# Kernel optimization log

Hardware: AMD Instinct MI355X
Metric: run time of the kernel (lower is better)

## Reference

```python
import jax, jax.numpy as jnp
import numpy as np

B, C_L_IN, C_L_OUT, C_J = 512, 64, 64, 16


def setup_inputs() -> dict:
    key = jax.random.key(0)
    ks = jax.random.split(key, 8)
    std = 0.02 / C_L_IN ** 0.5
    return {
        "F_in": jax.random.normal(ks[0], (B, C_L_IN, 4, 4), jnp.float32),
        "theta": jax.random.normal(ks[1], (B, C_J), jnp.float32),
        "W_bias": std * jax.random.normal(ks[2], (C_L_OUT, C_L_IN, 4, 4), jnp.float32),
        "W_cos": std * jax.random.normal(ks[3], (C_L_OUT, C_L_IN, C_J, 4, 4), jnp.float32),
        "W_sin": std * jax.random.normal(ks[4], (C_L_OUT, C_L_IN, C_J, 4, 4), jnp.float32),
        "Wb_bias": std * jax.random.normal(ks[5], (C_L_OUT, C_L_IN, 4, 4), jnp.float32),
        "Wb_cos": std * jax.random.normal(ks[6], (C_L_OUT, C_L_IN, C_J, 4, 4), jnp.float32),
        "Wb_sin": std * jax.random.normal(ks[7], (C_L_OUT, C_L_IN, C_J, 4, 4), jnp.float32),
    }


def reference(F_in, theta, W_bias, W_cos, W_sin, Wb_bias, Wb_cos, Wb_sin):
    cos_t = jnp.cos(theta)  # (B, C_J)
    sin_t = jnp.sin(theta)
    # U, Ub: (B, C_L_out, C_L_in, 4, 4)
    U = (W_bias
         + jnp.einsum('jicpq,bc->bjipq', W_cos, cos_t)
         + jnp.einsum('jicpq,bc->bjipq', W_sin, sin_t))
    Ub = (Wb_bias
          + jnp.einsum('jicpq,bc->bjipq', Wb_cos, cos_t)
          + jnp.einsum('jicpq,bc->bjipq', Wb_sin, sin_t))
    term1 = jnp.einsum('bipq,bjiqr->bjpr', F_in, U)
    term2 = jnp.einsum('bjipq,biqr->bjpr', Ub, F_in)
    return term1 + term2
```

## Files before the change

kernel.cpp:

```cpp
#include <hip/hip_runtime.h>


#define NRO_B   512
#define NRO_CL  64
#define K_DIM   8448
#define M_DIM   2048
#define N_DIM   256
#define SK      8
#define B_ELems  ((size_t)N_DIM * K_DIM)
#define FV_ELems ((size_t)M_DIM * N_DIM)
#define P_ELems  ((size_t)2 * SK * M_DIM * N_DIM)

typedef __attribute__((ext_vector_type(8))) _Float16 half8;
typedef __attribute__((ext_vector_type(4))) _Float16 half4_t;
typedef __attribute__((ext_vector_type(4))) float floatx4;

__device__ __forceinline__ void load16(const float* p, float w[4][4]) {
    const float4* p4 = (const float4*)p;
    #pragma unroll
    for (int a = 0; a < 4; ++a) {
        float4 x = p4[a];
        w[a][0] = x.x; w[a][1] = x.y; w[a][2] = x.z; w[a][3] = x.w;
    }
}

__device__ __forceinline__ half8 scale8(half8 v, _Float16 s) {
    half8 r;
    #pragma unroll
    for (int x = 0; x < 8; ++x) r[x] = v[x] * s;
    return r;
}

__global__ __launch_bounds__(256) void nro_prep(
    const float* __restrict__ F_in,
    const float* __restrict__ W_bias, const float* __restrict__ W_cos,
    const float* __restrict__ W_sin,  const float* __restrict__ Wb_bias,
    const float* __restrict__ Wb_cos, const float* __restrict__ Wb_sin,
    _Float16* __restrict__ Bbuf,
    _Float16* __restrict__ Fv)
{
    const int w = threadIdx.x >> 6, i = threadIdx.x & 63;
    if (blockIdx.x < 128) {
        const int b = blockIdx.x * 4 + w;
        float f[4][4];
        load16(F_in + ((size_t)b * 64 + i) * 16, f);
        #pragma unroll
        for (int a = 0; a < 4; ++a) {
            half4_t v0 = { (_Float16)f[a][0], (_Float16)f[a][1],
                           (_Float16)f[a][2], (_Float16)f[a][3] };
            *(half4_t*)(Fv + (size_t)(b * 4 + a) * 256 + i * 4) = v0;
            half4_t v1 = { (_Float16)f[0][a], (_Float16)f[1][a],
                           (_Float16)f[2][a], (_Float16)f[3][a] };
            *(half4_t*)(Fv + FV_ELems + (size_t)(b * 4 + a) * 256 + i * 4) = v1;
        }
    } else {
        const int unit = (blockIdx.x - 128) * 4 + w;
        const int j = unit >> 5, c = (unit >> 1) & 15, h = unit & 1;
        _Float16* Bd = Bbuf + (size_t)h * B_ELems;
        const size_t wbase = (((size_t)(j * 64 + i)) * 16 + c) * 16;

        float wc4[4][4], ws4[4][4];
        if (h == 0) { load16(W_cos  + wbase, wc4); load16(W_sin  + wbase, ws4); }
        else        { load16(Wb_cos + wbase, wc4); load16(Wb_sin + wbase, ws4); }

        const int gc  = (1 + c)  * 8 + (i >> 3);
        const int gs  = (17 + c) * 8 + (i >> 3);
        const int kin = (i & 7) * 4;
        #pragma unroll
        for (int a = 0; a < 4; ++a) {
            const int n = j * 4 + a;
            half4_t vc, vs;
            if (h == 0) {
                vc = (half4_t){ (_Float16)wc4[0][a], (_Float16)wc4[1][a],
                                (_Float16)wc4[2][a], (_Float16)wc4[3][a] };
                vs = (half4_t){ (_Float16)ws4[0][a], (_Float16)ws4[1][a],
                                (_Float16)ws4[2][a], (_Float16)ws4[3][a] };
            } else {
                vc = (half4_t){ (_Float16)wc4[a][0], (_Float16)wc4[a][1],
                                (_Float16)wc4[a][2], (_Float16)wc4[a][3] };
                vs = (half4_t){ (_Float16)ws4[a][0], (_Float16)ws4[a][1],
                                (_Float16)ws4[a][2], (_Float16)ws4[a][3] };
            }
            *(half4_t*)(Bd + ((size_t)gc * 256 + n) * 32 + kin) = vc;
            *(half4_t*)(Bd + ((size_t)gs * 256 + n) * 32 + kin) = vs;
        }
        if (c == 0) {
            float t[4][4];
            load16(((h == 0) ? W_bias : Wb_bias) + ((size_t)(j * 64 + i)) * 16, t);
            #pragma unroll
            for (int a = 0; a < 4; ++a) {
                half4_t v;
                if (h == 0) v = (half4_t){ (_Float16)t[0][a], (_Float16)t[1][a],
                                           (_Float16)t[2][a], (_Float16)t[3][a] };
                else        v = (half4_t){ (_Float16)t[a][0], (_Float16)t[a][1],
                                           (_Float16)t[a][2], (_Float16)t[a][3] };
                *(half4_t*)(Bd + ((size_t)(i >> 3) * 256 + (j * 4 + a)) * 32 + kin) = v;
            }
        }
    }
}

__global__ __launch_bounds__(512, 4) void nro_gemm(
    const _Float16* __restrict__ Bbuf, const _Float16* __restrict__ Fv,
    const float* __restrict__ theta,
    float* __restrict__ part)
{
    const int zs = blockIdx.x;
    const int z  = zs >> 3;
    const int sk = zs & 7;
    const int m0 = blockIdx.y * 128;

    const _Float16* Bm = Bbuf + (size_t)z * B_ELems;
    const _Float16* Fm = Fv + (size_t)z * FV_ELems + (size_t)m0 * 256;

    __shared__ _Float16 Fs[128 * 264];
    __shared__ float    trig[32 * 34];

    const int tid  = threadIdx.x;
    const int lane = tid & 63;
    const int w    = tid >> 6;
    const int wm   = (w >> 2) * 64;
    const int wn   = (w & 3) * 64;

    #pragma unroll
    for (int kk = 0; kk < 8; ++kk) {
        const int idx = kk * 512 + tid;
        const int row = idx >> 5, cf = idx & 31;
        half8 v = *(const half8*)(Fm + (size_t)row * 256 + cf * 8);
        *(half8*)(Fs + row * 264 + cf * 8) = v;
    }
    {
        const int bl = tid >> 4, c = tid & 15;
        const float th = theta[(m0 >> 2) * 16 + tid];
        trig[bl * 34 + 1 + c]  = __cosf(th);
        trig[bl * 34 + 17 + c] = __sinf(th);
        if (c == 0) trig[bl * 34] = 1.0f;
    }
    __syncthreads();

    const int fr = lane & 15, fq8 = (lane >> 4) * 8;

    const _Float16* Brow[4];
    #pragma unroll
    for (int t = 0; t < 4; ++t)
        Brow[t] = Bm + (size_t)(wn + t * 16 + fr) * 32 + fq8;

    floatx4 acc[4][4] = {};
    _Float16 tv[4] = {};

    int g = sk * 33;
    for (int kt = 0; kt < 33; ++kt, ++g) {
        const int cp  = g >> 3;
        const int iq0 = (g & 7) * 32;
        if (kt == 0 || (g & 7) == 0) {
            #pragma unroll
            for (int t = 0; t < 4; ++t)
                tv[t] = (_Float16)trig[((wm >> 2) + t * 4 + (fr >> 2)) * 34 + cp];
        }
        half8 bf[4];
        #pragma unroll
        for (int t = 0; t < 4; ++t)
            bf[t] = *(const half8*)(Brow[t] + (size_t)g * 8192);
        half8 af[4];
        #pragma unroll
        for (int t = 0; t < 4; ++t) {
            half8 fvf = *(const half8*)(Fs + (wm + t * 16 + fr) * 264 + iq0 + fq8);
            af[t] = scale8(fvf, tv[t]);
        }
        #pragma unroll
        for (int mt = 0; mt < 4; ++mt)
            #pragma unroll
            for (int nt = 0; nt < 4; ++nt)
                acc[mt][nt] = __builtin_amdgcn_mfma_f32_16x16x32_f16(
                    af[mt], bf[nt], acc[mt][nt], 0, 0, 0);
    }

    const int col = lane & 15, row4 = (lane >> 4) * 4;
    #pragma unroll
    for (int mt = 0; mt < 4; ++mt)
        #pragma unroll
        for (int nt = 0; nt < 4; ++nt)
            #pragma unroll
            for (int e = 0; e < 4; ++e) {
                const int m = m0 + wm + mt * 16 + row4 + e;
                const int n = wn + nt * 16 + col;
                part[((size_t)zs * M_DIM + m) * N_DIM + n] = acc[mt][nt][e];
            }
}

__global__ __launch_bounds__(256) void nro_reduce(
    const float* __restrict__ part, float* __restrict__ out)
{
    const int t = blockIdx.x * 256 + threadIdx.x;
    const int b = t >> 8;
    const int j = (t >> 2) & 63;
    const int p = t & 3;

    float4 o = make_float4(0.f, 0.f, 0.f, 0.f);
    #pragma unroll
    for (int sk = 0; sk < SK; ++sk) {
        const float4 c1 = *(const float4*)(
            part + ((size_t)sk * M_DIM + b * 4 + p) * N_DIM + j * 4);
        o.x += c1.x; o.y += c1.y; o.z += c1.z; o.w += c1.w;
        const float* p2 = part + ((size_t)(SK + sk) * M_DIM + b * 4) * N_DIM + j * 4 + p;
        o.x += p2[0 * N_DIM]; o.y += p2[1 * N_DIM];
        o.z += p2[2 * N_DIM]; o.w += p2[3 * N_DIM];
    }
    *(float4*)(out + ((size_t)(b * 64 + j) * 16 + p * 4)) = o;
}

__global__ __launch_bounds__(256, 2) void nro_fallback(
    const float* __restrict__ F_in, const float* __restrict__ theta,
    const float* __restrict__ W_bias, const float* __restrict__ W_cos,
    const float* __restrict__ W_sin,  const float* __restrict__ Wb_bias,
    const float* __restrict__ Wb_cos, const float* __restrict__ Wb_sin,
    float* __restrict__ out)
{
    __shared__ float smem[8448];
    const int j      = blockIdx.x >> 3;
    const int isplit = blockIdx.x & 7;
    const int i0     = isplit * 8;
    const int lane   = threadIdx.x & 63;
    const int chunk  = __builtin_amdgcn_readfirstlane(threadIdx.x >> 6);
    const int b      = blockIdx.y * 64 + lane;
    const int tid    = threadIdx.x;
    {
        float4* s4 = (float4*)smem;
        const int base16  = (j * 64 + i0) * 16;
        const int base256 = (j * 64 + i0) * 256;
        if (tid < 32)      s4[tid] = ((const float4*)(W_bias + base16))[tid];
        else if (tid < 64) s4[tid] = ((const float4*)(Wb_bias + base16))[tid - 32];
        #pragma unroll
        for (int r = 0; r < 2; ++r) {
            const int k = r * 256 + tid;
            s4[64 + k]   = ((const float4*)(W_cos  + base256))[k];
            s4[576 + k]  = ((const float4*)(W_sin  + base256))[k];
            s4[1088 + k] = ((const float4*)(Wb_cos + base256))[k];
            s4[1600 + k] = ((const float4*)(Wb_sin + base256))[k];
        }
    }
    float csc[16], css[16];
    #pragma unroll
    for (int c = 0; c < 16; ++c) {
        float t = theta[b * 16 + c];
        csc[c] = __cosf(t); css[c] = __sinf(t);
    }
    __syncthreads();
    float acc[16];
    #pragma unroll
    for (int e = 0; e < 16; ++e) acc[e] = 0.0f;
    #pragma unroll
    for (int ii = 0; ii < 2; ++ii) {
        const int il = chunk * 2 + ii;
        const int i  = i0 + il;
        float f[16];
        const float4* fp = (const float4*)(F_in + (b * 64 + i) * 16);
        #pragma unroll
        for (int v = 0; v < 4; ++v) {
            float4 x = fp[v];
            f[v*4+0]=x.x; f[v*4+1]=x.y; f[v*4+2]=x.z; f[v*4+3]=x.w;
        }
        const float* wb  = smem + il * 16;
        const float* wbb = smem + 128  + il * 16;
        const float* wc  = smem + 256  + il * 256;
        const float* wsn = smem + 2304 + il * 256;
        const float* wbc = smem + 4352 + il * 256;
        const float* wbs = smem + 6400 + il * 256;
        float U[16], Ub[16];
        #pragma unroll
        for (int e = 0; e < 16; ++e) { U[e] = wb[e]; Ub[e] = wbb[e]; }
        #pragma unroll 4
        for (int c = 0; c < 16; ++c) {
            const float cc = csc[c], ss = css[c];
            #pragma unroll
            for (int e = 0; e < 16; ++e) {
                U[e]  = fmaf(wc [c*16+e], cc, U[e]);
                U[e]  = fmaf(wsn[c*16+e], ss, U[e]);
                Ub[e] = fmaf(wbc[c*16+e], cc, Ub[e]);
                Ub[e] = fmaf(wbs[c*16+e], ss, Ub[e]);
            }
        }
        #pragma unroll
        for (int p = 0; p < 4; ++p)
            #pragma unroll
            for (int r = 0; r < 4; ++r) {
                float a = acc[p*4+r];
                #pragma unroll
                for (int q = 0; q < 4; ++q) {
                    a = fmaf(f[p*4+q],  U[q*4+r], a);
                    a = fmaf(Ub[p*4+q], f[q*4+r], a);
                }
                acc[p*4+r] = a;
            }
    }
    __syncthreads();
    if (chunk > 0) {
        float* r = smem + (chunk - 1) * 1088 + lane * 17;
        #pragma unroll
        for (int e = 0; e < 16; ++e) r[e] = acc[e];
    }
    __syncthreads();
    if (chunk == 0) {
        #pragma unroll
        for (int cc = 0; cc < 3; ++cc) {
            const float* r = smem + cc * 1088 + lane * 17;
            #pragma unroll
            for (int e = 0; e < 16; ++e) acc[e] += r[e];
        }
        float* o = out + ((size_t)b * 64 + j) * 16;
        #pragma unroll
        for (int e = 0; e < 16; ++e) atomicAdd(o + e, acc[e]);
    }
}

extern "C" void kernel_launch(void* const* d_in, const int* in_sizes, int n_in,
                              void* d_out, int out_size, void* d_ws, size_t ws_size,
                              hipStream_t stream) {
    const float* F_in    = (const float*)d_in[0];
    const float* theta   = (const float*)d_in[1];
    const float* W_bias  = (const float*)d_in[2];
    const float* W_cos   = (const float*)d_in[3];
    const float* W_sin   = (const float*)d_in[4];
    const float* Wb_bias = (const float*)d_in[5];
    const float* Wb_cos  = (const float*)d_in[6];
    const float* Wb_sin  = (const float*)d_in[7];
    float* out = (float*)d_out;

    const size_t needB  = 2 * B_ELems  * sizeof(_Float16);
    const size_t needFv = 2 * FV_ELems * sizeof(_Float16);
    const size_t needP  = P_ELems * sizeof(float);
    if (ws_size >= needB + needFv + needP) {
        _Float16* Bbuf = (_Float16*)d_ws;
        _Float16* Fv   = (_Float16*)((char*)d_ws + needB);
        float*    part = (float*)((char*)d_ws + needB + needFv);
        nro_prep<<<640, 256, 0, stream>>>(F_in, W_bias, W_cos, W_sin,
                                          Wb_bias, Wb_cos, Wb_sin, Bbuf, Fv);
        nro_gemm<<<dim3(16, 16), 512, 0, stream>>>(Bbuf, Fv, theta, part);
        nro_reduce<<<512, 256, 0, stream>>>(part, out);
    } else {
        hipMemsetAsync(out, 0, (size_t)out_size * sizeof(float), stream);
        dim3 grid(64 * 8, 512 / 64, 1);
        nro_fallback<<<grid, 256, 0, stream>>>(
            F_in, theta, W_bias, W_cos, W_sin, Wb_bias, Wb_cos, Wb_sin, out);
    }
}
```

Before: 111.5 us.

## Halve GEMM block M-tile and double-buffer B fragment loads in registers

The GEMM block tile shrinks from 128 to 64 rows with 4 waves instead of 8, doubling the grid to 512 blocks and halving shared memory per block. The K loop is unrolled by two, with B fragments for the next two chunks prefetched into registers while the current chunks run their MFMAs. The aim is to hide global-load latency behind MFMA work and to spread the work across more CUs. In exchange, each B tile is reloaded by twice as many blocks, and the extra prefetch registers raise register pressure.

```diff
diff --git a/kernel.cpp b/kernel.cpp
--- a/kernel.cpp
+++ b/kernel.cpp
@@ -100,7 +100,7 @@
     }
 }
 
-__global__ __launch_bounds__(512, 4) void nro_gemm(
+__global__ __launch_bounds__(256, 2) void nro_gemm(
     const _Float16* __restrict__ Bbuf, const _Float16* __restrict__ Fv,
     const float* __restrict__ theta,
     float* __restrict__ part)
@@ -108,23 +108,22 @@
     const int zs = blockIdx.x;
     const int z  = zs >> 3;
     const int sk = zs & 7;
-    const int m0 = blockIdx.y * 128;
+    const int m0 = blockIdx.y * 64;
 
     const _Float16* Bm = Bbuf + (size_t)z * B_ELems;
     const _Float16* Fm = Fv + (size_t)z * FV_ELems + (size_t)m0 * 256;
 
-    __shared__ _Float16 Fs[128 * 264];
-    __shared__ float    trig[32 * 34];
+    __shared__ _Float16 Fs[64 * 264];
+    __shared__ float    trig[16 * 34];
 
     const int tid  = threadIdx.x;
     const int lane = tid & 63;
     const int w    = tid >> 6;
-    const int wm   = (w >> 2) * 64;
-    const int wn   = (w & 3) * 64;
+    const int wn   = w * 64;
 
     #pragma unroll
     for (int kk = 0; kk < 8; ++kk) {
-        const int idx = kk * 512 + tid;
+        const int idx = kk * 256 + tid;
         const int row = idx >> 5, cf = idx & 31;
         half8 v = *(const half8*)(Fm + (size_t)row * 256 + cf * 8);
         *(half8*)(Fs + row * 264 + cf * 8) = v;
@@ -147,33 +146,63 @@
 
     floatx4 acc[4][4] = {};
     _Float16 tv[4] = {};
-
-    int g = sk * 33;
-    for (int kt = 0; kt < 33; ++kt, ++g) {
-        const int cp  = g >> 3;
-        const int iq0 = (g & 7) * 32;
-        if (kt == 0 || (g & 7) == 0) {
+    int cp_last = -1;
+
+    const int base = sk * 33;
+    half8 q0[4], q1[4];
+    #pragma unroll
+    for (int t = 0; t < 4; ++t) {
+        q0[t] = *(const half8*)(Brow[t] + (size_t)(base + 0) * 8192);
+        q1[t] = *(const half8*)(Brow[t] + (size_t)(base + 1) * 8192);
+    }
+
+    #define NRO_CHUNK(GABS, QREG)                                             \
+        {                                                                     \
+            const int cp_ = (GABS) >> 3;                                      \
+            if (cp_ != cp_last) {                                             \
+                cp_last = cp_;                                                \
+                _Pragma("unroll")                                             \
+                for (int t = 0; t < 4; ++t)                                   \
+                    tv[t] = (_Float16)trig[(t * 4 + (fr >> 2)) * 34 + cp_];   \
+            }                                                                 \
+            const int iq0_ = ((GABS) & 7) * 32;                               \
+            half8 af[4];                                                      \
+            _Pragma("unroll")                                                 \
+            for (int t = 0; t < 4; ++t) {                                     \
+                half8 fvf = *(const half8*)(Fs + (t * 16 + fr) * 264          \
+                                            + iq0_ + fq8);                    \
+                af[t] = scale8(fvf, tv[t]);                                   \
+            }                                                                 \
+            _Pragma("unroll")                                                 \
+            for (int mt = 0; mt < 4; ++mt)                                    \
+                _Pragma("unroll")                                             \
+                for (int nt = 0; nt < 4; ++nt)                                \
+                    acc[mt][nt] = __builtin_amdgcn_mfma_f32_16x16x32_f16(     \
+                        af[mt], QREG[nt], acc[mt][nt], 0, 0, 0);              \
+        }
+
+    for (int it = 0; it < 16; ++it) {
+        const int c0 = base + 2 * it;
+        half8 p0[4], p1[4];
+        #pragma unroll
+        for (int t = 0; t < 4; ++t)
+            p0[t] = *(const half8*)(Brow[t] + (size_t)(c0 + 2) * 8192);
+        if (it < 15) {
             #pragma unroll
             for (int t = 0; t < 4; ++t)
-                tv[t] = (_Float16)trig[((wm >> 2) + t * 4 + (fr >> 2)) * 34 + cp];
-        }
-        half8 bf[4];
-        #pragma unroll
-        for (int t = 0; t < 4; ++t)
-            bf[t] = *(const half8*)(Brow[t] + (size_t)g * 8192);
-        half8 af[4];
-        #pragma unroll
-        for (int t = 0; t < 4; ++t) {
-            half8 fvf = *(const half8*)(Fs + (wm + t * 16 + fr) * 264 + iq0 + fq8);
-            af[t] = scale8(fvf, tv[t]);
-        }
-        #pragma unroll
-        for (int mt = 0; mt < 4; ++mt)
-            #pragma unroll
-            for (int nt = 0; nt < 4; ++nt)
-                acc[mt][nt] = __builtin_amdgcn_mfma_f32_16x16x32_f16(
-                    af[mt], bf[nt], acc[mt][nt], 0, 0, 0);
-    }
+                p1[t] = *(const half8*)(Brow[t] + (size_t)(c0 + 3) * 8192);
+        }
+        NRO_CHUNK(c0, q0);
+        NRO_CHUNK(c0 + 1, q1);
+        #pragma unroll
+        for (int t = 0; t < 4; ++t) q0[t] = p0[t];
+        if (it < 15) {
+            #pragma unroll
+            for (int t = 0; t < 4; ++t) q1[t] = p1[t];
+        }
+    }
+    NRO_CHUNK(base + 32, q0);
+    #undef NRO_CHUNK
 
     const int col = lane & 15, row4 = (lane >> 4) * 4;
     #pragma unroll
@@ -182,7 +211,7 @@
         for (int nt = 0; nt < 4; ++nt)
             #pragma unroll
             for (int e = 0; e < 4; ++e) {
-                const int m = m0 + wm + mt * 16 + row4 + e;
+                const int m = m0 + mt * 16 + row4 + e;
                 const int n = wn + nt * 16 + col;
                 part[((size_t)zs * M_DIM + m) * N_DIM + n] = acc[mt][nt][e];
             }
@@ -335,7 +364,7 @@
         float*    part = (float*)((char*)d_ws + needB + needFv);
         nro_prep<<<640, 256, 0, stream>>>(F_in, W_bias, W_cos, W_sin,
                                           Wb_bias, Wb_cos, Wb_sin, Bbuf, Fv);
-        nro_gemm<<<dim3(16, 16), 512, 0, stream>>>(Bbuf, Fv, theta, part);
+        nro_gemm<<<dim3(16, 32), 256, 0, stream>>>(Bbuf, Fv, theta, part);
         nro_reduce<<<512, 256, 0, stream>>>(part, out);
     } else {
         hipMemsetAsync(out, 0, (size_t)out_size * sizeof(float), stream);
```

Measured after the change: 110.2 us. No clear change (-1.2%).
